# Optimization experiments

Measured on AMD Instinct MI355X. Metric: run time of the kernel, lower is better.

Reference implementation:

```python
import jax, jax.numpy as jnp
import numpy as np

B, T, E = 8, 1024, 512
H = 1024            # hidden_dim
NH, QD, VD = 4, 256, 512
C1, C2 = 512, 2     # conv1_out, conv2_out
K, PAD = 3, 1


def conv1d(x, w, b, pad):
    # x: [B, Cin, T], w: [Cout, Cin, K]
    y = jax.lax.conv_general_dilated(x, w, (1,), [(pad, pad)],
                                     dimension_numbers=('NCH', 'OIH', 'NCH'))
    return y + b[None, :, None]


def setup_inputs() -> dict:
    key = jax.random.key(0)
    ks = jax.random.split(key, 24)
    n = lambda i, shape, s=0.02: jax.random.normal(ks[i], shape, dtype=jnp.float32) * s
    inp = {
        'x':    jax.random.normal(ks[0], (B, T, E), dtype=jnp.float32),
        # in_pro: two 1x1 convs over channels (acting as linears)
        'w_in1': n(1, (E, E)), 'b_in1': jnp.zeros((E,), jnp.float32),
        'w_in2': n(2, (E, E)), 'b_in2': jnp.zeros((E,), jnp.float32),
        # attention projections
        'w_q': n(3, (NH * QD, E), float(np.sqrt(2.0 / (E + QD)))), 'b_q': jnp.zeros((NH * QD,), jnp.float32),
        'w_k': n(4, (NH * QD, E), float(np.sqrt(2.0 / (E + QD)))), 'b_k': jnp.zeros((NH * QD,), jnp.float32),
        'w_v': n(5, (NH * VD, E), float(np.sqrt(2.0 / (E + VD)))), 'b_v': jnp.zeros((NH * VD,), jnp.float32),
        # output projection (1x1 conv)
        'w_p': n(6, (E, NH * VD)), 'b_p': jnp.zeros((E,), jnp.float32),
        # layernorm
        'ln_g': jnp.ones((E,), jnp.float32), 'ln_b': jnp.zeros((E,), jnp.float32),
        # LSTM (1 layer, unidirectional, hidden H)
        'w_ih': n(7, (4 * H, E)), 'w_hh': n(8, (4 * H, H)),
        'b_ih': jnp.zeros((4 * H,), jnp.float32), 'b_hh': jnp.zeros((4 * H,), jnp.float32),
        # attention pooling convs
        'w_c1': n(9, (C1, H, K)), 'b_c1': jnp.zeros((C1,), jnp.float32),
        'w_c2': n(10, (C2, C1, K)), 'b_c2': jnp.zeros((C2,), jnp.float32),
    }
    return inp


def reference(x, w_in1, b_in1, w_in2, b_in2, w_q, b_q, w_k, b_k, w_v, b_v,
              w_p, b_p, ln_g, ln_b, w_ih, w_hh, b_ih, b_hh,
              w_c1, b_c1, w_c2, b_c2):
    # in_pro: 1x1 conv -> LeakyReLU(0.25) -> 1x1 conv (channel-wise linears)
    h = jnp.einsum('bte,fe->btf', x, w_in1) + b_in1
    h = jnp.where(h >= 0, h, 0.25 * h)
    h = jnp.einsum('bte,fe->btf', h, w_in2) + b_in2  # [B,T,E]

    # multi-head attention (no scale factor, as in the source)
    q = (jnp.einsum('bte,fe->btf', h, w_q) + b_q).reshape(B, T, NH, QD)
    k = (jnp.einsum('bte,fe->btf', h, w_k) + b_k).reshape(B, T, NH, QD)
    v = (jnp.einsum('bte,fe->btf', h, w_v) + b_v).reshape(B, T, NH, VD)
    scores = jnp.einsum('btnd,bsnd->bnts', q, k)          # [B,NH,T,T]
    attn = jax.nn.softmax(scores, axis=-1)
    o = jnp.einsum('bnts,bsnd->btnd', attn, v)            # [B,T,NH,VD]
    o = o.reshape(B, T, NH * VD)

    # p_conv1 (1x1) then LayerNorm over E
    y = jnp.einsum('btc,ec->bte', o, w_p) + b_p           # [B,T,E]
    mu = jnp.mean(y, axis=-1, keepdims=True)
    var = jnp.mean(jnp.square(y - mu), axis=-1, keepdims=True)
    y = (y - mu) * jax.lax.rsqrt(var + 1e-5) * ln_g + ln_b

    # LSTM (batch_first, 1 layer); dropout is identity in eval mode
    def step(carry, xt):
        hprev, cprev = carry
        g = xt @ w_ih.T + hprev @ w_hh.T + b_ih + b_hh    # [B,4H]
        i, f, gg, og = jnp.split(g, 4, axis=-1)
        c = jax.nn.sigmoid(f) * cprev + jax.nn.sigmoid(i) * jnp.tanh(gg)
        hn = jax.nn.sigmoid(og) * jnp.tanh(c)
        return (hn, c), hn
    init = (jnp.zeros((B, H), y.dtype), jnp.zeros((B, H), y.dtype))
    _, hs = jax.lax.scan(step, init, jnp.swapaxes(y, 0, 1))  # [T,B,H]
    lstm_out = jnp.swapaxes(hs, 0, 1)                        # [B,T,H]

    # conv-based attention pooling
    a = conv1d(jnp.swapaxes(lstm_out, 1, 2), w_c1, b_c1, PAD)  # [B,C1,T]
    a = jax.nn.relu(a)
    a = conv1d(a, w_c2, b_c2, PAD)                              # [B,C2,T]
    a = jax.nn.softmax(a, axis=2)
    feat = jnp.einsum('bct,bth->bch', a, lstm_out)              # [B,C2,H]
    return feat.reshape(B, C2 * H)
```

## Files before the change

### kernel.cpp

```cpp
#include <hip/hip_runtime.h>
#include <stdint.h>

typedef short short8 __attribute__((ext_vector_type(8)));
typedef short short4v __attribute__((ext_vector_type(4)));
typedef float float4v __attribute__((ext_vector_type(4)));

__device__ __forceinline__ float b2f(short s) {
    return __uint_as_float(((unsigned)(unsigned short)s) << 16);
}
__device__ __forceinline__ short f2b(float f) {
    unsigned u = __float_as_uint(f);
    unsigned r = (u + 0x7fffu + ((u >> 16) & 1u)) >> 16;
    return (short)r;
}

__global__ void k_cvt_all(const float4v* __restrict__ xs,
                          const float4v* __restrict__ s0, const float4v* __restrict__ s1,
                          const float4v* __restrict__ s2, const float4v* __restrict__ s3,
                          const float4v* __restrict__ s4, const float4v* __restrict__ s5,
                          const float4v* __restrict__ s6, const float4v* __restrict__ s7,
                          short4v* __restrict__ xq, short4v* __restrict__ wq) {
    int i = blockIdx.x * blockDim.x + threadIdx.x;
    int stride = gridDim.x * blockDim.x;
    for (; i < 3538944; i += stride) {
        float4v v;
        short4v* dst;
        int di;
        if (i < 1048576) { v = xs[i]; dst = xq; di = i; }
        else {
            int j = i - 1048576;
            dst = wq; di = j;
            if      (j <   65536) v = s0[j];
            else if (j <  131072) v = s1[j -   65536];
            else if (j <  262144) v = s2[j -  131072];
            else if (j <  393216) v = s3[j -  262144];
            else if (j <  655360) v = s4[j -  393216];
            else if (j <  917504) v = s5[j -  655360];
            else if (j < 1441792) v = s6[j -  917504];
            else                  v = s7[j - 1441792];
        }
        short4v o;
        o[0] = f2b(v[0]); o[1] = f2b(v[1]); o[2] = f2b(v[2]); o[3] = f2b(v[3]);
        dst[di] = o;
    }
}

__global__ void k_small_prep(const float* __restrict__ wc1, short* __restrict__ wc1b,
                             const float* __restrict__ bih, const float* __restrict__ bhh,
                             float* __restrict__ bsum, short* __restrict__ lpad,
                             short* __restrict__ hs0, short* __restrict__ hs1,
                             int* __restrict__ arr, const float* __restrict__ bc2,
                             float* __restrict__ a2) {
    int t0 = blockIdx.x * blockDim.x + threadIdx.x;
    int stride = gridDim.x * blockDim.x;
    for (int i = t0; i < 512 * 3072; i += stride) {
        int c = i / 3072, rr = i % 3072, dk = rr / 1024, h = rr % 1024;
        wc1b[i] = f2b(wc1[(c * 1024 + h) * 3 + dk]);
    }
    for (int i = t0; i < 4096; i += stride) bsum[i] = bih[i] + bhh[i];
    for (int i = t0; i < 16 * 1024; i += stride) {
        int b = i >> 11, r = (i >> 10) & 1, h = i & 1023;
        lpad[((long)(b * 1026 + r * 1025)) * 1024 + h] = 0;
    }
    for (int i = t0; i < 16384; i += stride) { hs0[i] = 0; hs1[i] = 0; }
    for (int i = t0; i < 64; i += stride) arr[i] = 0;
    for (int i = t0; i < 16384; i += stride) a2[i] = bc2[(i >> 10) & 1];
}

__global__ __launch_bounds__(256) void k_gemm_bt(
    const short* __restrict__ A, const short* __restrict__ B,
    float* __restrict__ Cf, short* __restrict__ Cb,
    const float* __restrict__ bias,
    int M, int N, int K, int lda, int ldb, int ldc,
    int z0n, long sA0, long sA1, long sB0, long sB1, long sC0, long sC1,
    int act, int gap, const float* __restrict__ bias2, int nsplit)
{
    __shared__ __align__(16) short lds[2 * 128 * 32];
    const int z = blockIdx.z;
    const int z0 = z % z0n, z1 = z / z0n;
    A += z1 * sA1 + z0 * sA0;
    B += z1 * sB1 + z0 * sB0;
    const long coff = z1 * sC1 + z0 * sC0;
    const int tn0 = blockIdx.x * 128, tm0 = blockIdx.y * 128;
    const int tid = threadIdx.x, ln = tid & 63, wv = tid >> 6;
    const int wr = wv >> 1, wc = wv & 1;

    const short* gbase[4];
    {
        const int gcol = (ln & 3) ^ ((ln >> 3) & 3);
#pragma unroll
        for (int j = 0; j < 4; ++j) {
            int c = wv * 4 + j;
            if (c < 8) {
                long grow = (long)(tm0 + c * 16 + (ln >> 2));
                if (gap) grow += 2 * (grow >> 10);
                gbase[j] = A + grow * (long)lda + gcol * 8;
            } else {
                gbase[j] = B + (long)(tn0 + (c - 8) * 16 + (ln >> 2)) * ldb + gcol * 8;
            }
        }
    }

    float4v acc[4][4];
#pragma unroll
    for (int i = 0; i < 4; ++i)
#pragma unroll
        for (int j = 0; j < 4; ++j) acc[i][j] = (float4v){0.f, 0.f, 0.f, 0.f};

    const int nk = K >> 5;
    for (int kt = 0; kt < nk; ++kt) {
        __syncthreads();
#pragma unroll
        for (int j = 0; j < 4; ++j) {
            int c = wv * 4 + j;
            __builtin_amdgcn_global_load_lds(
                (const __attribute__((address_space(1))) void*)(gbase[j] + kt * 32),
                (__attribute__((address_space(3))) void*)((short8*)lds + c * 64),
                16, 0, 0);
        }
        __syncthreads();

        short8 af[4], bf_[4];
        const int q = ln >> 4;
#pragma unroll
        for (int i = 0; i < 4; ++i) {
            int r = wr * 64 + i * 16 + (ln & 15);
            af[i] = ((short8*)lds)[r * 4 + (q ^ ((r >> 1) & 3))];
        }
#pragma unroll
        for (int j = 0; j < 4; ++j) {
            int r = wc * 64 + j * 16 + (ln & 15);
            bf_[j] = ((short8*)lds)[512 + r * 4 + (q ^ ((r >> 1) & 3))];
        }
#pragma unroll
        for (int i = 0; i < 4; ++i)
#pragma unroll
            for (int j = 0; j < 4; ++j)
                acc[i][j] = __builtin_amdgcn_mfma_f32_16x16x32_bf16(af[i], bf_[j], acc[i][j], 0, 0, 0);
    }

#pragma unroll
    for (int j = 0; j < 4; ++j) {
        int nglob = tn0 + wc * 64 + j * 16 + (ln & 15);
        float bv = 0.f;
        if (bias) bv = (bias2 && nglob >= nsplit) ? bias2[nglob - nsplit] : bias[nglob];
#pragma unroll
        for (int i = 0; i < 4; ++i) {
#pragma unroll
            for (int r = 0; r < 4; ++r) {
                int mglob = tm0 + wr * 64 + i * 16 + (ln >> 4) * 4 + r;
                float v = acc[i][j][r] + bv;
                if (act == 1) v = (v >= 0.f) ? v : 0.25f * v;
                else if (act == 2) v = fmaxf(v, 0.f);
                long ci = coff + (long)mglob * ldc + nglob;
                if (Cf) Cf[ci] = v;
                if (Cb) Cb[ci] = f2b(v);
            }
        }
    }
}

__global__ __launch_bounds__(256) void k_gemm_bt64(
    const short* __restrict__ A, const short* __restrict__ B,
    float* __restrict__ Cf, short* __restrict__ Cb,
    const float* __restrict__ bias,
    int M, int N, int K, int lda, int ldb, int ldc,
    int z0n, long sA0, long sA1, long sB0, long sB1, long sC0, long sC1,
    int act, int gap, const float* __restrict__ bias2, int nsplit)
{
    __shared__ __align__(16) short lds[(64 + 128) * 32];
    const int z = blockIdx.z;
    const int z0 = z % z0n, z1 = z / z0n;
    A += z1 * sA1 + z0 * sA0;
    B += z1 * sB1 + z0 * sB0;
    const long coff = z1 * sC1 + z0 * sC0;
    const int tn0 = blockIdx.x * 128, tm0 = blockIdx.y * 64;
    const int tid = threadIdx.x, ln = tid & 63, wv = tid >> 6;
    const int wr = wv >> 1, wc = wv & 1;

    const short* gbase[3];
    {
        const int gcol = (ln & 3) ^ ((ln >> 3) & 3);
#pragma unroll
        for (int j = 0; j < 3; ++j) {
            int c = wv * 3 + j;
            if (c < 4) {
                long grow = (long)(tm0 + c * 16 + (ln >> 2));
                if (gap) grow += 2 * (grow >> 10);
                gbase[j] = A + grow * (long)lda + gcol * 8;
            } else {
                gbase[j] = B + (long)(tn0 + (c - 4) * 16 + (ln >> 2)) * ldb + gcol * 8;
            }
        }
    }

    float4v acc[2][4];
#pragma unroll
    for (int i = 0; i < 2; ++i)
#pragma unroll
        for (int j = 0; j < 4; ++j) acc[i][j] = (float4v){0.f, 0.f, 0.f, 0.f};

    const int nk = K >> 5;
    for (int kt = 0; kt < nk; ++kt) {
        __syncthreads();
#pragma unroll
        for (int j = 0; j < 3; ++j) {
            int c = wv * 3 + j;
            __builtin_amdgcn_global_load_lds(
                (const __attribute__((address_space(1))) void*)(gbase[j] + kt * 32),
                (__attribute__((address_space(3))) void*)((short8*)lds + c * 64),
                16, 0, 0);
        }
        __syncthreads();

        short8 af[2], bf_[4];
        const int q = ln >> 4;
#pragma unroll
        for (int i = 0; i < 2; ++i) {
            int r = wr * 32 + i * 16 + (ln & 15);
            af[i] = ((short8*)lds)[r * 4 + (q ^ ((r >> 1) & 3))];
        }
#pragma unroll
        for (int j = 0; j < 4; ++j) {
            int r = wc * 64 + j * 16 + (ln & 15);
            bf_[j] = ((short8*)lds)[256 + r * 4 + (q ^ ((r >> 1) & 3))];
        }
#pragma unroll
        for (int i = 0; i < 2; ++i)
#pragma unroll
            for (int j = 0; j < 4; ++j)
                acc[i][j] = __builtin_amdgcn_mfma_f32_16x16x32_bf16(af[i], bf_[j], acc[i][j], 0, 0, 0);
    }

#pragma unroll
    for (int j = 0; j < 4; ++j) {
        int nglob = tn0 + wc * 64 + j * 16 + (ln & 15);
        float bv = 0.f;
        if (bias) bv = (bias2 && nglob >= nsplit) ? bias2[nglob - nsplit] : bias[nglob];
#pragma unroll
        for (int i = 0; i < 2; ++i) {
#pragma unroll
            for (int r = 0; r < 4; ++r) {
                int mglob = tm0 + wr * 32 + i * 16 + (ln >> 4) * 4 + r;
                float v = acc[i][j][r] + bv;
                if (act == 1) v = (v >= 0.f) ? v : 0.25f * v;
                else if (act == 2) v = fmaxf(v, 0.f);
                long ci = coff + (long)mglob * ldc + nglob;
                if (Cf) Cf[ci] = v;
                if (Cb) Cb[ci] = f2b(v);
            }
        }
    }
}

__global__ __launch_bounds__(256) void k_comb1(const float4v* __restrict__ p0,
                                               const float4v* __restrict__ p1,
                                               const float* __restrict__ bias,
                                               short4v* __restrict__ o) {
    int i = blockIdx.x * blockDim.x + threadIdx.x;
    int stride = gridDim.x * blockDim.x;
    for (; i < 1048576; i += stride) {
        float4v a = p0[i], b = p1[i];
        short4v r;
#pragma unroll
        for (int u = 0; u < 4; ++u) {
            float v = a[u] + b[u] + bias[(i * 4 + u) & 511];
            r[u] = f2b(fmaxf(v, 0.f));
        }
        o[i] = r;
    }
}

__global__ __launch_bounds__(256) void k_softmax_rows_bf16(short* __restrict__ p) {
    long row = blockIdx.x;
    short* r = p + (row << 10);
    int tid = threadIdx.x;
    float v[4];
    float mx = -3.4e38f;
#pragma unroll
    for (int i = 0; i < 4; ++i) { v[i] = b2f(r[tid + (i << 8)]); mx = fmaxf(mx, v[i]); }
#pragma unroll
    for (int d = 32; d > 0; d >>= 1) mx = fmaxf(mx, __shfl_down(mx, d));
    __shared__ float red[4], red2[4];
    if ((tid & 63) == 0) red[tid >> 6] = mx;
    __syncthreads();
    mx = fmaxf(fmaxf(red[0], red[1]), fmaxf(red[2], red[3]));
    float s = 0.f;
#pragma unroll
    for (int i = 0; i < 4; ++i) { v[i] = __expf(v[i] - mx); s += v[i]; }
#pragma unroll
    for (int d = 32; d > 0; d >>= 1) s += __shfl_down(s, d);
    if ((tid & 63) == 0) red2[tid >> 6] = s;
    __syncthreads();
    s = red2[0] + red2[1] + red2[2] + red2[3];
    float inv = 1.f / s;
#pragma unroll
    for (int i = 0; i < 4; ++i) r[tid + (i << 8)] = f2b(v[i] * inv);
}

__global__ __launch_bounds__(256) void k_layernorm(const short* __restrict__ y,
                                                   const float* __restrict__ gam,
                                                   const float* __restrict__ bet,
                                                   short* __restrict__ o) {
    const long row = blockIdx.x;
    const short* r = y + (row << 9);
    const int tid = threadIdx.x;
    float v0 = b2f(r[tid]), v1 = b2f(r[tid + 256]);
    float s = v0 + v1, ss = v0 * v0 + v1 * v1;
#pragma unroll
    for (int d = 32; d > 0; d >>= 1) { s += __shfl_down(s, d); ss += __shfl_down(ss, d); }
    __shared__ float rs_[4], rss[4];
    if ((tid & 63) == 0) { rs_[tid >> 6] = s; rss[tid >> 6] = ss; }
    __syncthreads();
    s = rs_[0] + rs_[1] + rs_[2] + rs_[3];
    ss = rss[0] + rss[1] + rss[2] + rss[3];
    float mean = s * (1.f / 512.f);
    float var = ss * (1.f / 512.f) - mean * mean;
    float rstd = rsqrtf(var + 1e-5f);
    short* out = o + (row << 9);
    out[tid]       = f2b((v0 - mean) * rstd * gam[tid]       + bet[tid]);
    out[tid + 256] = f2b((v1 - mean) * rstd * gam[tid + 256] + bet[tid + 256]);
}

__global__ __launch_bounds__(256) void k_vT(const short* __restrict__ v, short* __restrict__ vT) {
    __shared__ short t[32][34];
    int bn = blockIdx.z, b = bn >> 2, n = bn & 3;
    int s0 = blockIdx.y * 32, d0 = blockIdx.x * 32;
    int lx = threadIdx.x & 31, ly = threadIdx.x >> 5;
#pragma unroll
    for (int i = 0; i < 4; ++i) {
        int s = ly + i * 8;
        t[s][lx] = v[(long)(b * 1024 + s0 + s) * 2048 + n * 512 + d0 + lx];
    }
    __syncthreads();
#pragma unroll
    for (int i = 0; i < 4; ++i) {
        int d = ly + i * 8;
        vT[((long)bn * 512 + d0 + d) * 1024 + s0 + lx] = t[lx][d];
    }
}

__global__ __launch_bounds__(256) void k_lstm(
    const short* __restrict__ whh, const short* __restrict__ igb,
    short* __restrict__ hA, short* __restrict__ hB,
    short* __restrict__ lstm_pad, int* __restrict__ arr)
{
    const int g = blockIdx.x;
    const int tid = threadIdx.x;
    const int ln = tid & 63, wv = tid >> 6;
    const int kbase = wv * 256 + ((ln >> 4) << 3);
    const int arow = ln & 15;

    short8 wf[4][8];
#pragma unroll
    for (int q = 0; q < 4; ++q) {
        long row = (long)q * 1024 + g * 16 + (ln & 15);
#pragma unroll
        for (int kk = 0; kk < 8; ++kk)
            wf[q][kk] = *(const short8*)&whh[row * 1024 + kbase + kk * 32];
    }

    __shared__ float part[4][16][68];
    const int gm = tid >> 4, gu = tid & 15;
    float c_prev = 0.f;
    float igv[4];
    if (tid < 128) {
#pragma unroll
        for (int q = 0; q < 4; ++q)
            igv[q] = b2f(igb[((long)gm * 1024 + 0) * 4096 + q * 1024 + g * 16 + gu]);
    }

    for (int step = 0; step < 1024; ++step) {
        const short* hp = (step & 1) ? hB : hA;
        short8 af[8];
        if (arow < 8) {
            const unsigned long long* hq =
                (const unsigned long long*)(hp + arow * 1024 + kbase);
#pragma unroll
            for (int kk = 0; kk < 8; ++kk) {
                union { unsigned long long u[2]; short8 s; } cv;
                cv.u[0] = __hip_atomic_load(hq + kk * 8,     __ATOMIC_RELAXED, __HIP_MEMORY_SCOPE_AGENT);
                cv.u[1] = __hip_atomic_load(hq + kk * 8 + 1, __ATOMIC_RELAXED, __HIP_MEMORY_SCOPE_AGENT);
                af[kk] = cv.s;
            }
        } else {
#pragma unroll
            for (int kk = 0; kk < 8; ++kk) af[kk] = (short8){0, 0, 0, 0, 0, 0, 0, 0};
        }

        float4v acc[4];
#pragma unroll
        for (int q = 0; q < 4; ++q) acc[q] = (float4v){0.f, 0.f, 0.f, 0.f};
#pragma unroll
        for (int kk = 0; kk < 8; ++kk)
#pragma unroll
            for (int q = 0; q < 4; ++q)
                acc[q] = __builtin_amdgcn_mfma_f32_16x16x32_bf16(af[kk], wf[q][kk], acc[q], 0, 0, 0);

#pragma unroll
        for (int q = 0; q < 4; ++q)
#pragma unroll
            for (int rr = 0; rr < 4; ++rr)
                part[wv][(ln >> 4) * 4 + rr][q * 16 + (ln & 15)] = acc[q][rr];
        __syncthreads();

        if (tid < 128) {
            float psum[4];
#pragma unroll
            for (int q = 0; q < 4; ++q)
                psum[q] = part[0][gm][q * 16 + gu] + part[1][gm][q * 16 + gu]
                        + part[2][gm][q * 16 + gu] + part[3][gm][q * 16 + gu];
            float g0 = psum[0] + igv[0];
            float g1 = psum[1] + igv[1];
            float g2 = psum[2] + igv[2];
            float g3 = psum[3] + igv[3];
            float iv = 1.f / (1.f + __expf(-g0));
            float fv = 1.f / (1.f + __expf(-g1));
            float gv = 2.f / (1.f + __expf(-2.f * g2)) - 1.f;
            float ov = 1.f / (1.f + __expf(-g3));
            float c = fv * c_prev + iv * gv;
            c_prev = c;
            float h = ov * (2.f / (1.f + __expf(-2.f * c)) - 1.f);
            short hb16 = f2b(h);
            short* hn = (step & 1) ? hA : hB;
            __hip_atomic_store(&hn[gm * 1024 + g * 16 + gu], hb16,
                               __ATOMIC_RELAXED, __HIP_MEMORY_SCOPE_AGENT);
            lstm_pad[((long)gm * 1026 + step + 1) * 1024 + g * 16 + gu] = hb16;
        }

        __syncthreads();
        if (tid == 0)
            __hip_atomic_store(&arr[g], step + 1, __ATOMIC_RELAXED, __HIP_MEMORY_SCOPE_AGENT);
        if (tid < 128 && step + 1 < 1024) {
#pragma unroll
            for (int q = 0; q < 4; ++q)
                igv[q] = b2f(igb[((long)gm * 1024 + step + 1) * 4096 + q * 1024 + g * 16 + gu]);
        }
        if (wv == 0) {
            const int target = step + 1;
            long att = 0;
            while (true) {
                int f0 = __hip_atomic_load(&arr[ln], __ATOMIC_RELAXED, __HIP_MEMORY_SCOPE_AGENT);
                if (__all(f0 >= target)) break;
                if (++att > 20000000L) break;
                __builtin_amdgcn_s_sleep(1);
            }
        }
        __syncthreads();
    }
}

__global__ __launch_bounds__(256) void k_conv2(const short* __restrict__ a1,
                                               const float* __restrict__ w,
                                               float* __restrict__ a2,
                                               float* __restrict__ dz) {
    __shared__ float wl[384];
    int blk = blockIdx.x;
    int chunk = blk & 3, tq = (blk >> 2) & 3, bc = blk >> 4;
    int b = bc >> 1, c = bc & 1, t0 = tq * 256;
    int tid = threadIdx.x;
    int gid = blk * 256 + tid;
    if (gid < 16384) dz[gid] = 0.f;
    for (int i = tid; i < 384; i += 256) wl[i] = w[c * 1536 + chunk * 384 + i];
    __syncthreads();
    int t = t0 + tid;
    int j0 = chunk * 16;
    float s = 0.f;
    for (int dk = 0; dk < 3; ++dk) {
        int tt = t + dk - 1;
        if (tt < 0 || tt >= 1024) continue;
        const short8* arow = (const short8*)(a1 + (long)(b * 1024 + tt) * 512);
#pragma unroll 4
        for (int j = 0; j < 16; ++j) {
            short8 v = arow[j0 + j];
#pragma unroll
            for (int u = 0; u < 8; ++u)
                s += b2f(v[u]) * wl[(j * 8 + u) * 3 + dk];
        }
    }
    atomicAdd(&a2[(b * 2 + c) * 1024 + t], s);
}

__global__ __launch_bounds__(256) void k_feat(const float* __restrict__ a2,
                                              const short* __restrict__ lstm_pad,
                                              float* __restrict__ out) {
    int blk = blockIdx.x;
    int tc = blk & 3, qh = (blk >> 2) & 3, bc = blk >> 4;
    int b = bc >> 1;
    int tid = threadIdx.x;
    int h = qh * 256 + tid;
    __shared__ float aws[256];
    __shared__ float red[4], red2[4];
    float v[4];
    float mx = -3.4e38f;
#pragma unroll
    for (int i = 0; i < 4; ++i) { v[i] = a2[bc * 1024 + tid + (i << 8)]; mx = fmaxf(mx, v[i]); }
#pragma unroll
    for (int d = 32; d > 0; d >>= 1) mx = fmaxf(mx, __shfl_down(mx, d));
    if ((tid & 63) == 0) red[tid >> 6] = mx;
    __syncthreads();
    mx = fmaxf(fmaxf(red[0], red[1]), fmaxf(red[2], red[3]));
    float s = 0.f;
#pragma unroll
    for (int i = 0; i < 4; ++i) { v[i] = __expf(v[i] - mx); s += v[i]; }
#pragma unroll
    for (int d = 32; d > 0; d >>= 1) s += __shfl_down(s, d);
    if ((tid & 63) == 0) red2[tid >> 6] = s;
    __syncthreads();
    s = red2[0] + red2[1] + red2[2] + red2[3];
    float inv = 1.f / s;
    aws[tid] = v[tc] * inv;
    __syncthreads();
    float acc = 0.f;
#pragma unroll 16
    for (int j = 0; j < 256; ++j)
        acc += aws[j] * b2f(lstm_pad[((long)(b * 1026 + tc * 256 + j + 1)) * 1024 + h]);
    atomicAdd(&out[bc * 1024 + h], acc);
}

static void gemm_bt(hipStream_t st, const short* A, const short* B, float* Cf, short* Cb,
                    const float* bias, int M, int N, int K, int lda, int ldb, int ldc,
                    int z, int z0n, long sA0, long sA1, long sB0, long sB1, long sC0, long sC1,
                    int act, int gap, const float* bias2 = nullptr, int nsplit = 0) {
    dim3 grid(N / 128, M / 128, z);
    k_gemm_bt<<<grid, dim3(256), 0, st>>>(A, B, Cf, Cb, bias, M, N, K, lda, ldb, ldc,
                                          z0n, sA0, sA1, sB0, sB1, sC0, sC1, act, gap, bias2, nsplit);
}

static void gemm_bt64(hipStream_t st, const short* A, const short* B, float* Cf, short* Cb,
                      const float* bias, int M, int N, int K, int lda, int ldb, int ldc,
                      int z, int z0n, long sA0, long sA1, long sB0, long sB1, long sC0, long sC1,
                      int act, int gap, const float* bias2 = nullptr, int nsplit = 0) {
    dim3 grid(N / 128, M / 64, z);
    k_gemm_bt64<<<grid, dim3(256), 0, st>>>(A, B, Cf, Cb, bias, M, N, K, lda, ldb, ldc,
                                            z0n, sA0, sA1, sB0, sB1, sC0, sC1, act, gap, bias2, nsplit);
}

extern "C" void kernel_launch(void* const* d_in, const int* in_sizes, int n_in,
                              void* d_out, int out_size, void* d_ws, size_t ws_size,
                              hipStream_t stream) {
    if (ws_size < 199409920u) return;

    const float* x     = (const float*)d_in[0];
    const float* w_in1 = (const float*)d_in[1];
    const float* b_in1 = (const float*)d_in[2];
    const float* w_in2 = (const float*)d_in[3];
    const float* b_in2 = (const float*)d_in[4];
    const float* w_q   = (const float*)d_in[5];
    const float* b_q   = (const float*)d_in[6];
    const float* w_k   = (const float*)d_in[7];
    const float* b_k   = (const float*)d_in[8];
    const float* w_v   = (const float*)d_in[9];
    const float* b_v   = (const float*)d_in[10];
    const float* w_p   = (const float*)d_in[11];
    const float* b_p   = (const float*)d_in[12];
    const float* ln_g  = (const float*)d_in[13];
    const float* ln_b  = (const float*)d_in[14];
    const float* w_ih  = (const float*)d_in[15];
    const float* w_hh  = (const float*)d_in[16];
    const float* b_ih  = (const float*)d_in[17];
    const float* b_hh  = (const float*)d_in[18];
    const float* w_c1  = (const float*)d_in[19];
    const float* b_c1  = (const float*)d_in[20];
    const float* w_c2  = (const float*)d_in[21];
    const float* b_c2  = (const float*)d_in[22];

    char* ws = (char*)d_ws;
    short* w1b  = (short*)(ws + 0);
    short* w2b  = (short*)(ws + 524288);
    short* wqb  = (short*)(ws + 1048576);
    short* wvb  = (short*)(ws + 3145728);
    short* wpb  = (short*)(ws + 5242880);
    short* wihb = (short*)(ws + 7340032);
    short* whhb = (short*)(ws + 11534336);
    short* wc1b = (short*)(ws + 19922944);
    float* bsum = (float*)(ws + 23068672);
    short* hs0  = (short*)(ws + 23085056);
    short* hs1  = (short*)(ws + 23117824);
    int*   arr  = (int*)  (ws + 23150592);
    float* a2   = (float*)(ws + 23150848);
    short* lpad = (short*)(ws + 23216384);
    const size_t D0 = 40026368u;
    short* xbf   = (short*)(ws + D0);
    short* h1bf  = (short*)(ws + D0 + 8388608);
    short* h2bf  = (short*)(ws + D0 + 16777216);
    short* qkC   = (short*)(ws + D0 + 25165824);
    short* vbf   = (short*)(ws + D0 + 58720256);
    short* vTbf  = (short*)(ws + D0 + 92274688);
    short* scb   = (short*)(ws + D0 + 58720256);
    short* obf   = (short*)(ws + D0 + 125829120);
    short* ybf   = (short*)(ws + D0 + 58720256);
    short* ylnbf = (short*)(ws + D0 + 67108864);
    short* igb   = (short*)(ws + D0 + 92274688);
    short* a1bf  = (short*)(ws + D0);
    float* cp0   = (float*)(ws + D0 + 8388608);
    float* cp1   = (float*)(ws + D0 + 25165824);

    k_cvt_all<<<dim3(4096), dim3(256), 0, stream>>>(
        (const float4v*)x,
        (const float4v*)w_in1, (const float4v*)w_in2, (const float4v*)w_q, (const float4v*)w_k,
        (const float4v*)w_v, (const float4v*)w_p, (const float4v*)w_ih, (const float4v*)w_hh,
        (short4v*)xbf, (short4v*)w1b);
    k_small_prep<<<dim3(128), dim3(256), 0, stream>>>(
        w_c1, wc1b, b_ih, b_hh, bsum, lpad, hs0, hs1, arr, b_c2, a2);

    gemm_bt64(stream, xbf, w1b, nullptr, h1bf, b_in1, 8192, 512, 512, 512, 512, 512,
              1, 1, 0, 0, 0, 0, 0, 0, 1, 0);
    gemm_bt64(stream, h1bf, w2b, nullptr, h2bf, b_in2, 8192, 512, 512, 512, 512, 512,
              1, 1, 0, 0, 0, 0, 0, 0, 0, 0);
    gemm_bt(stream, h2bf, wqb, nullptr, qkC, b_q, 8192, 2048, 512, 512, 512, 2048,
            1, 1, 0, 0, 0, 0, 0, 0, 0, 0, b_k, 1024);
    gemm_bt(stream, h2bf, wvb, nullptr, vbf, b_v, 8192, 2048, 512, 512, 512, 2048,
            1, 1, 0, 0, 0, 0, 0, 0, 0, 0);
    k_vT<<<dim3(16, 32, 32), dim3(256), 0, stream>>>(vbf, vTbf);

    for (int bg = 0; bg < 2; ++bg) {
        const short* qb = qkC + (long)bg * 8388608;
        const short* kb = qkC + 1024 + (long)bg * 8388608;
        gemm_bt(stream, qb, kb, nullptr, scb, nullptr, 1024, 1024, 256, 2048, 2048, 1024,
                16, 4, 256, 2097152, 256, 2097152, 1048576, 4194304, 0, 0);
        k_softmax_rows_bf16<<<dim3(16384), dim3(256), 0, stream>>>(scb);
        gemm_bt64(stream, scb, vTbf + (long)bg * 8388608, nullptr, obf + (long)bg * 8388608, nullptr,
                  1024, 512, 1024, 1024, 1024, 2048,
                  16, 4, 1048576, 4194304, 524288, 2097152, 512, 2097152, 0, 0);
    }

    gemm_bt64(stream, obf, wpb, nullptr, ybf, b_p, 8192, 512, 2048, 2048, 2048, 512,
              1, 1, 0, 0, 0, 0, 0, 0, 0, 0);
    k_layernorm<<<dim3(8192), dim3(256), 0, stream>>>(ybf, ln_g, ln_b, ylnbf);
    gemm_bt(stream, ylnbf, wihb, nullptr, igb, bsum, 8192, 4096, 512, 512, 512, 4096,
            1, 1, 0, 0, 0, 0, 0, 0, 0, 0);
    k_lstm<<<dim3(64), dim3(256), 0, stream>>>(whhb, igb, hs0, hs1, lpad, arr);
    gemm_bt64(stream, lpad, wc1b, cp0, nullptr, nullptr, 8192, 512, 1536, 1024, 3072, 512,
              2, 2, 1536, 0, 1536, 0, 4194304, 0, 0, 1);
    k_comb1<<<dim3(4096), dim3(256), 0, stream>>>(
        (const float4v*)cp0, (const float4v*)cp1, b_c1, (short4v*)a1bf);
    k_conv2<<<dim3(256), dim3(256), 0, stream>>>(a1bf, w_c2, a2, (float*)d_out);
    k_feat<<<dim3(256), dim3(256), 0, stream>>>(a2, lpad, (float*)d_out);
    (void)in_sizes; (void)n_in; (void)out_size; (void)ws_size;
}
```

Measured before the change: 3.905 ms.

## Fuse QKV projections into one GEMM writing V transposed directly

Merges the separate Q/K and V projection GEMMs into a single GEMM over a concatenated weight (the bf16 weight buffers are already contiguous) with a concatenated bias buffer. The V-part tiles write their output transposed per head straight into the vT layout, which removes the standalone transpose kernel and the intermediate V buffer round trip. It also merges the two prep kernels into one launch. In exchange the transposed epilogue stores are strided short4 writes rather than row-contiguous stores.

```diff
diff --git a/kernel.cpp b/kernel.cpp
--- a/kernel.cpp
+++ b/kernel.cpp
@@ -14,15 +14,24 @@
     return (short)r;
 }
 
-__global__ void k_cvt_all(const float4v* __restrict__ xs,
-                          const float4v* __restrict__ s0, const float4v* __restrict__ s1,
-                          const float4v* __restrict__ s2, const float4v* __restrict__ s3,
-                          const float4v* __restrict__ s4, const float4v* __restrict__ s5,
-                          const float4v* __restrict__ s6, const float4v* __restrict__ s7,
-                          short4v* __restrict__ xq, short4v* __restrict__ wq) {
-    int i = blockIdx.x * blockDim.x + threadIdx.x;
+__global__ void k_prep_all(const float4v* __restrict__ xs,
+                           const float4v* __restrict__ s0, const float4v* __restrict__ s1,
+                           const float4v* __restrict__ s2, const float4v* __restrict__ s3,
+                           const float4v* __restrict__ s4, const float4v* __restrict__ s5,
+                           const float4v* __restrict__ s6, const float4v* __restrict__ s7,
+                           short4v* __restrict__ xq, short4v* __restrict__ wq,
+                           const float* __restrict__ wc1, short* __restrict__ wc1b,
+                           const float* __restrict__ bih, const float* __restrict__ bhh,
+                           float* __restrict__ bsum,
+                           const float* __restrict__ bq, const float* __restrict__ bk,
+                           const float* __restrict__ bv, float* __restrict__ bqkv,
+                           short* __restrict__ lpad,
+                           short* __restrict__ hs0, short* __restrict__ hs1,
+                           int* __restrict__ arr, const float* __restrict__ bc2,
+                           float* __restrict__ a2) {
+    int t0 = blockIdx.x * blockDim.x + threadIdx.x;
     int stride = gridDim.x * blockDim.x;
-    for (; i < 3538944; i += stride) {
+    for (int i = t0; i < 3538944; i += stride) {
         float4v v;
         short4v* dst;
         int di;
@@ -43,21 +52,18 @@
         o[0] = f2b(v[0]); o[1] = f2b(v[1]); o[2] = f2b(v[2]); o[3] = f2b(v[3]);
         dst[di] = o;
     }
-}
-
-__global__ void k_small_prep(const float* __restrict__ wc1, short* __restrict__ wc1b,
-                             const float* __restrict__ bih, const float* __restrict__ bhh,
-                             float* __restrict__ bsum, short* __restrict__ lpad,
-                             short* __restrict__ hs0, short* __restrict__ hs1,
-                             int* __restrict__ arr, const float* __restrict__ bc2,
-                             float* __restrict__ a2) {
-    int t0 = blockIdx.x * blockDim.x + threadIdx.x;
-    int stride = gridDim.x * blockDim.x;
     for (int i = t0; i < 512 * 3072; i += stride) {
         int c = i / 3072, rr = i % 3072, dk = rr / 1024, h = rr % 1024;
         wc1b[i] = f2b(wc1[(c * 1024 + h) * 3 + dk]);
     }
     for (int i = t0; i < 4096; i += stride) bsum[i] = bih[i] + bhh[i];
+    for (int i = t0; i < 4096; i += stride) {
+        float v;
+        if (i < 1024) v = bq[i];
+        else if (i < 2048) v = bk[i - 1024];
+        else v = bv[i - 2048];
+        bqkv[i] = v;
+    }
     for (int i = t0; i < 16 * 1024; i += stride) {
         int b = i >> 11, r = (i >> 10) & 1, h = i & 1023;
         lpad[((long)(b * 1026 + r * 1025)) * 1024 + h] = 0;
@@ -73,7 +79,7 @@
     const float* __restrict__ bias,
     int M, int N, int K, int lda, int ldb, int ldc,
     int z0n, long sA0, long sA1, long sB0, long sB1, long sC0, long sC1,
-    int act, int gap, const float* __restrict__ bias2, int nsplit)
+    int act, int gap, short* __restrict__ Cvt, int vtn0)
 {
     __shared__ __align__(16) short lds[2 * 128 * 32];
     const int z = blockIdx.z;
@@ -139,11 +145,30 @@
                 acc[i][j] = __builtin_amdgcn_mfma_f32_16x16x32_bf16(af[i], bf_[j], acc[i][j], 0, 0, 0);
     }
 
+    if (Cvt && tn0 >= vtn0) {
+#pragma unroll
+        for (int j = 0; j < 4; ++j) {
+            int nglob = tn0 + wc * 64 + j * 16 + (ln & 15);
+            float bv = bias ? bias[nglob] : 0.f;
+            int nv = nglob - vtn0;
+            int nn = nv >> 9, d = nv & 511;
+#pragma unroll
+            for (int i = 0; i < 4; ++i) {
+                int m0 = tm0 + wr * 64 + i * 16 + (ln >> 4) * 4;
+                int b = m0 >> 10, s = m0 & 1023;
+                short4v pk;
+#pragma unroll
+                for (int r = 0; r < 4; ++r) pk[r] = f2b(acc[i][j][r] + bv);
+                *(short4v*)&Cvt[((long)((b * 4 + nn) * 512 + d)) * 1024 + s] = pk;
+            }
+        }
+        return;
+    }
+
 #pragma unroll
     for (int j = 0; j < 4; ++j) {
         int nglob = tn0 + wc * 64 + j * 16 + (ln & 15);
-        float bv = 0.f;
-        if (bias) bv = (bias2 && nglob >= nsplit) ? bias2[nglob - nsplit] : bias[nglob];
+        float bv = bias ? bias[nglob] : 0.f;
 #pragma unroll
         for (int i = 0; i < 4; ++i) {
 #pragma unroll
@@ -166,7 +191,7 @@
     const float* __restrict__ bias,
     int M, int N, int K, int lda, int ldb, int ldc,
     int z0n, long sA0, long sA1, long sB0, long sB1, long sC0, long sC1,
-    int act, int gap, const float* __restrict__ bias2, int nsplit)
+    int act, int gap)
 {
     __shared__ __align__(16) short lds[(64 + 128) * 32];
     const int z = blockIdx.z;
@@ -235,8 +260,7 @@
 #pragma unroll
     for (int j = 0; j < 4; ++j) {
         int nglob = tn0 + wc * 64 + j * 16 + (ln & 15);
-        float bv = 0.f;
-        if (bias) bv = (bias2 && nglob >= nsplit) ? bias2[nglob - nsplit] : bias[nglob];
+        float bv = bias ? bias[nglob] : 0.f;
 #pragma unroll
         for (int i = 0; i < 2; ++i) {
 #pragma unroll
@@ -320,24 +344,6 @@
     short* out = o + (row << 9);
     out[tid]       = f2b((v0 - mean) * rstd * gam[tid]       + bet[tid]);
     out[tid + 256] = f2b((v1 - mean) * rstd * gam[tid + 256] + bet[tid + 256]);
-}
-
-__global__ __launch_bounds__(256) void k_vT(const short* __restrict__ v, short* __restrict__ vT) {
-    __shared__ short t[32][34];
-    int bn = blockIdx.z, b = bn >> 2, n = bn & 3;
-    int s0 = blockIdx.y * 32, d0 = blockIdx.x * 32;
-    int lx = threadIdx.x & 31, ly = threadIdx.x >> 5;
-#pragma unroll
-    for (int i = 0; i < 4; ++i) {
-        int s = ly + i * 8;
-        t[s][lx] = v[(long)(b * 1024 + s0 + s) * 2048 + n * 512 + d0 + lx];
-    }
-    __syncthreads();
-#pragma unroll
-    for (int i = 0; i < 4; ++i) {
-        int d = ly + i * 8;
-        vT[((long)bn * 512 + d0 + d) * 1024 + s0 + lx] = t[lx][d];
-    }
 }
 
 __global__ __launch_bounds__(256) void k_lstm(
@@ -521,19 +527,19 @@
 static void gemm_bt(hipStream_t st, const short* A, const short* B, float* Cf, short* Cb,
                     const float* bias, int M, int N, int K, int lda, int ldb, int ldc,
                     int z, int z0n, long sA0, long sA1, long sB0, long sB1, long sC0, long sC1,
-                    int act, int gap, const float* bias2 = nullptr, int nsplit = 0) {
+                    int act, int gap, short* Cvt = nullptr, int vtn0 = 0) {
     dim3 grid(N / 128, M / 128, z);
     k_gemm_bt<<<grid, dim3(256), 0, st>>>(A, B, Cf, Cb, bias, M, N, K, lda, ldb, ldc,
-                                          z0n, sA0, sA1, sB0, sB1, sC0, sC1, act, gap, bias2, nsplit);
+                                          z0n, sA0, sA1, sB0, sB1, sC0, sC1, act, gap, Cvt, vtn0);
 }
 
 static void gemm_bt64(hipStream_t st, const short* A, const short* B, float* Cf, short* Cb,
                       const float* bias, int M, int N, int K, int lda, int ldb, int ldc,
                       int z, int z0n, long sA0, long sA1, long sB0, long sB1, long sC0, long sC1,
-                      int act, int gap, const float* bias2 = nullptr, int nsplit = 0) {
+                      int act, int gap) {
     dim3 grid(N / 128, M / 64, z);
     k_gemm_bt64<<<grid, dim3(256), 0, st>>>(A, B, Cf, Cb, bias, M, N, K, lda, ldb, ldc,
-                                            z0n, sA0, sA1, sB0, sB1, sC0, sC1, act, gap, bias2, nsplit);
+                                            z0n, sA0, sA1, sB0, sB1, sC0, sC1, act, gap);
 }
 
 extern "C" void kernel_launch(void* const* d_in, const int* in_sizes, int n_in,
@@ -569,7 +575,6 @@
     short* w1b  = (short*)(ws + 0);
     short* w2b  = (short*)(ws + 524288);
     short* wqb  = (short*)(ws + 1048576);
-    short* wvb  = (short*)(ws + 3145728);
     short* wpb  = (short*)(ws + 5242880);
     short* wihb = (short*)(ws + 7340032);
     short* whhb = (short*)(ws + 11534336);
@@ -585,7 +590,7 @@
     short* h1bf  = (short*)(ws + D0 + 8388608);
     short* h2bf  = (short*)(ws + D0 + 16777216);
     short* qkC   = (short*)(ws + D0 + 25165824);
-    short* vbf   = (short*)(ws + D0 + 58720256);
+    float* bqkv  = (float*)(ws + D0 + 58720256);
     short* vTbf  = (short*)(ws + D0 + 92274688);
     short* scb   = (short*)(ws + D0 + 58720256);
     short* obf   = (short*)(ws + D0 + 125829120);
@@ -596,23 +601,20 @@
     float* cp0   = (float*)(ws + D0 + 8388608);
     float* cp1   = (float*)(ws + D0 + 25165824);
 
-    k_cvt_all<<<dim3(4096), dim3(256), 0, stream>>>(
+    k_prep_all<<<dim3(4096), dim3(256), 0, stream>>>(
         (const float4v*)x,
         (const float4v*)w_in1, (const float4v*)w_in2, (const float4v*)w_q, (const float4v*)w_k,
         (const float4v*)w_v, (const float4v*)w_p, (const float4v*)w_ih, (const float4v*)w_hh,
-        (short4v*)xbf, (short4v*)w1b);
-    k_small_prep<<<dim3(128), dim3(256), 0, stream>>>(
-        w_c1, wc1b, b_ih, b_hh, bsum, lpad, hs0, hs1, arr, b_c2, a2);
+        (short4v*)xbf, (short4v*)w1b,
+        w_c1, wc1b, b_ih, b_hh, bsum, b_q, b_k, b_v, bqkv,
+        lpad, hs0, hs1, arr, b_c2, a2);
 
     gemm_bt64(stream, xbf, w1b, nullptr, h1bf, b_in1, 8192, 512, 512, 512, 512, 512,
               1, 1, 0, 0, 0, 0, 0, 0, 1, 0);
     gemm_bt64(stream, h1bf, w2b, nullptr, h2bf, b_in2, 8192, 512, 512, 512, 512, 512,
               1, 1, 0, 0, 0, 0, 0, 0, 0, 0);
-    gemm_bt(stream, h2bf, wqb, nullptr, qkC, b_q, 8192, 2048, 512, 512, 512, 2048,
-            1, 1, 0, 0, 0, 0, 0, 0, 0, 0, b_k, 1024);
-    gemm_bt(stream, h2bf, wvb, nullptr, vbf, b_v, 8192, 2048, 512, 512, 512, 2048,
-            1, 1, 0, 0, 0, 0, 0, 0, 0, 0);
-    k_vT<<<dim3(16, 32, 32), dim3(256), 0, stream>>>(vbf, vTbf);
+    gemm_bt(stream, h2bf, wqb, nullptr, qkC, bqkv, 8192, 4096, 512, 512, 512, 2048,
+            1, 1, 0, 0, 0, 0, 0, 0, 0, 0, vTbf, 2048);
 
     for (int bg = 0; bg < 2; ++bg) {
         const short* qb = qkC + (long)bg * 8388608;
```

Result: no change. 3.873 ms (median of 3 runs) (-0.8%).
